# Kernel tuning notes

Measured on AMD Instinct MI355X. Metric: run time of the kernel, lower is better.

Reference implementation:

```python
import jax, jax.numpy as jnp
import numpy as np

B, N, D = 256, 400, 512
K = 20  # args.gcn_topk == self.k


def setup_inputs() -> dict:
    key = jax.random.key(0)
    k1, k2, k3, k4 = jax.random.split(key, 4)
    node_embs = jax.random.normal(k1, (B, N, D), dtype=jnp.float32)
    h_t = jax.random.normal(k2, (B, D), dtype=jnp.float32)
    mask = jnp.ones((B, N), dtype=jnp.float32)  # unused by forward, kept for signature fidelity
    # mapper = Linear(rnn_dim=512, gcn_dim=512) followed by Tanh
    lim = 1.0 / np.sqrt(D)
    W_map = jax.random.uniform(k3, (D, D), dtype=jnp.float32, minval=-lim, maxval=lim)
    b_map = jax.random.uniform(k4, (D,), dtype=jnp.float32, minval=-lim, maxval=lim)
    return {"node_embs": node_embs, "mask": mask, "h_t": h_t, "W_map": W_map, "b_map": b_map}


def reference(node_embs, mask, h_t, W_map, b_map):
    # scorer = Tanh(Linear(h_t.detach()))  -> [B, D]
    scorer = jnp.tanh(jax.lax.stop_gradient(h_t) @ W_map.T + b_map)
    # scores = bmm(node_embs, scorer) / ||scorer||  -> [B, N]
    scores = jnp.einsum('bnd,bd->bn', node_embs, scorer)
    scores = scores / jnp.linalg.norm(scorer, axis=1, keepdims=True)
    # top-k over nodes
    vals, topk_indices = jax.lax.top_k(scores, K)  # [B, K]
    # vals are always finite => topk_indices_out == topk_indices;
    # repeat_num = K/K + 1 = 2, then truncated back to K => no-op
    topk_indices_out = topk_indices
    # gather rows topk_indices; the original expand(-1,-1,gcn_topk) selects only
    # the FIRST K feature columns -> out is [B, K, K]
    gathered = jnp.take_along_axis(node_embs[:, :, :K], topk_indices[:, :, None], axis=1)
    tanh_s = jnp.tanh(jnp.take_along_axis(scores, topk_indices, axis=1))  # [B, K]
    out = gathered * tanh_s[:, :, None]  # [B, K, K]
    # softmax over nodes, entropy of the categorical, log-prob gather
    logp = jax.nn.log_softmax(scores, axis=1)  # [B, N]
    probs = jnp.exp(logp)
    entropy_object = -jnp.sum(probs * logp, axis=1)  # [B]
    score = jnp.take_along_axis(logp, topk_indices, axis=-1)  # [B, K]
    policy_score = jnp.mean(score, axis=1)  # [B]
    return (jnp.swapaxes(out, 1, 2), policy_score, scorer, entropy_object, topk_indices_out)
```

## Files before the change

kernel.cpp:

```cpp
#include <hip/hip_runtime.h>
#include <math.h>
#include <float.h>

#define BB 256
#define NN 400
#define DD 512
#define KK 20

__device__ __forceinline__ float dot8(float4 a0, float4 a1, float4 b0, float4 b1) {
    return a0.x*b0.x + a0.y*b0.y + a0.z*b0.z + a0.w*b0.w
         + a1.x*b1.x + a1.y*b1.y + a1.z*b1.z + a1.w*b1.w;
}

__global__ __launch_bounds__(1024) void scorer_kernel(
    const float* __restrict__ h_t,
    const float* __restrict__ W,
    const float* __restrict__ bmap,
    float* __restrict__ out2)
{
    const int blk = blockIdx.x;
    const int dc = blk & 15, bg = blk >> 4;
    const int wave = threadIdx.x >> 6, lane = threadIdx.x & 63;

    const int d0 = dc * 32 + wave * 2;
    const int d1 = d0 + 1;
    const float4* wp0 = (const float4*)(W + (size_t)d0 * DD);
    const float4* wp1 = (const float4*)(W + (size_t)d1 * DD);
    const float4 w00 = wp0[lane], w01 = wp0[lane + 64];
    const float4 w10 = wp1[lane], w11 = wp1[lane + 64];
    const float bias0 = bmap[d0], bias1 = bmap[d1];

    #pragma unroll 4
    for (int bi = 0; bi < 32; ++bi) {
        const int b = bg * 32 + bi;
        const float4* hp = (const float4*)(h_t + (size_t)b * DD);
        float4 hb0 = hp[lane], hb1 = hp[lane + 64];
        float p0 = dot8(w00, w01, hb0, hb1);
        float p1 = dot8(w10, w11, hb0, hb1);
        #pragma unroll
        for (int off = 32; off; off >>= 1) {
            p0 += __shfl_xor(p0, off, 64);
            p1 += __shfl_xor(p1, off, 64);
        }
        if (lane == 0) {
            out2[(size_t)b * DD + d0] = tanhf(p0 + bias0);
            out2[(size_t)b * DD + d1] = tanhf(p1 + bias1);
        }
    }
}

__global__ __launch_bounds__(1024, 4) void fused_topk_kernel(
    const float* __restrict__ embs,
    const float* __restrict__ scorer,
    float* __restrict__ out0,
    float* __restrict__ out1,
    float* __restrict__ out3,
    float* __restrict__ out4)
{
    const int b = blockIdx.x;
    const int t = threadIdx.x;
    const int wave = t >> 6, lane = t & 63;

    __shared__ float sh_sc[DD];
    __shared__ float sh_s[NN];
    __shared__ float redf[16], redf2[16], redq[8];
    __shared__ float mZ[3];
    __shared__ int   sh_topk[KK];
    __shared__ float sh_th[KK];

    if (t < DD) {
        float v = scorer[(size_t)b * DD + t];
        sh_sc[t] = v;
        float ss = v * v;
        #pragma unroll
        for (int off = 32; off; off >>= 1) ss += __shfl_xor(ss, off, 64);
        if (lane == 0) redq[wave] = ss;
    }
    __syncthreads();

    const float4 g0 = ((const float4*)sh_sc)[lane];
    const float4 g1 = ((const float4*)sh_sc)[lane + 64];

    {
        const int n0 = wave * 25;
        const float* base = embs + ((size_t)b * NN + n0) * DD;

        float4 A0[5], A1[5], B0[5], B1[5];
        #pragma unroll
        for (int r = 0; r < 5; ++r) {
            const float4* p = (const float4*)(base + (size_t)r * DD);
            A0[r] = p[lane]; A1[r] = p[lane + 64];
        }
        #pragma unroll
        for (int g = 0; g < 5; ++g) {
            if (g < 4) {
                #pragma unroll
                for (int r = 0; r < 5; ++r) {
                    const float4* p = (const float4*)(base + (size_t)((g + 1) * 5 + r) * DD);
                    B0[r] = p[lane]; B1[r] = p[lane + 64];
                }
            }
            float s[5];
            #pragma unroll
            for (int r = 0; r < 5; ++r) s[r] = dot8(A0[r], A1[r], g0, g1);
            #pragma unroll
            for (int off = 32; off; off >>= 1) {
                #pragma unroll
                for (int r = 0; r < 5; ++r) s[r] += __shfl_xor(s[r], off, 64);
            }
            if (lane == 0) {
                float* o = sh_s + n0 + g * 5;
                #pragma unroll
                for (int r = 0; r < 5; ++r) o[r] = s[r];
            }
            if (g < 4) {
                #pragma unroll
                for (int r = 0; r < 5; ++r) { A0[r] = B0[r]; A1[r] = B1[r]; }
            }
        }
    }
    __syncthreads();

    if (t == 0) {
        float tot = 0.f;
        #pragma unroll
        for (int i = 0; i < 8; ++i) tot += redq[i];
        mZ[0] = 1.0f / sqrtf(tot);
    }
    __syncthreads();
    const float inv = mZ[0];

    const float x = (t < NN) ? sh_s[t] * inv : -FLT_MAX;
    {
        float m = x;
        #pragma unroll
        for (int off = 32; off; off >>= 1) m = fmaxf(m, __shfl_xor(m, off, 64));
        if (lane == 0) redf[wave] = m;
    }
    __syncthreads();
    if (t == 0) {
        float m = redf[0];
        #pragma unroll
        for (int i = 1; i < 16; ++i) m = fmaxf(m, redf[i]);
        mZ[1] = m;
    }
    __syncthreads();
    const float m = mZ[1];

    {
        float e = 0.f, wv = 0.f;
        if (t < NN) {
            float d = x - m;
            e = expf(d);
            wv = e * d;
        }
        #pragma unroll
        for (int off = 32; off; off >>= 1) {
            e  += __shfl_xor(e, off, 64);
            wv += __shfl_xor(wv, off, 64);
        }
        if (lane == 0) { redf[wave] = e; redf2[wave] = wv; }
    }
    __syncthreads();
    if (t == 0) {
        float Z = 0.f, Ws = 0.f;
        #pragma unroll
        for (int i = 0; i < 16; ++i) { Z += redf[i]; Ws += redf2[i]; }
        float logZ = logf(Z);
        mZ[2] = logZ;
        out3[b] = logZ - Ws / Z;
    }
    __syncthreads();
    const float logZ = mZ[2];

    if (wave == 0) {
        float v0 = sh_s[lane      ] * inv;
        float v1 = sh_s[lane +  64] * inv;
        float v2 = sh_s[lane + 128] * inv;
        float v3 = sh_s[lane + 192] * inv;
        float v4 = sh_s[lane + 256] * inv;
        float v5 = sh_s[lane + 320] * inv;
        float v6 = (lane + 384 < NN) ? sh_s[lane + 384] * inv : -FLT_MAX;
        float acc = 0.f;
        for (int k = 0; k < KK; ++k) {
            float bv = v0; int bi = lane;
            if (v1 > bv) { bv = v1; bi = lane + 64; }
            if (v2 > bv) { bv = v2; bi = lane + 128; }
            if (v3 > bv) { bv = v3; bi = lane + 192; }
            if (v4 > bv) { bv = v4; bi = lane + 256; }
            if (v5 > bv) { bv = v5; bi = lane + 320; }
            if (v6 > bv) { bv = v6; bi = lane + 384; }
            #pragma unroll
            for (int off = 32; off; off >>= 1) {
                float ov = __shfl_xor(bv, off, 64);
                int   oi = __shfl_xor(bi, off, 64);
                if (ov > bv || (ov == bv && oi < bi)) { bv = ov; bi = oi; }
            }
            if (lane == 0) {
                sh_topk[k] = bi;
                sh_th[k] = tanhf(bv);
                out4[(size_t)b * KK + k] = (float)bi;
                acc += bv - m - logZ;
            }
            v0 = (bi == lane      ) ? -FLT_MAX : v0;
            v1 = (bi == lane +  64) ? -FLT_MAX : v1;
            v2 = (bi == lane + 128) ? -FLT_MAX : v2;
            v3 = (bi == lane + 192) ? -FLT_MAX : v3;
            v4 = (bi == lane + 256) ? -FLT_MAX : v4;
            v5 = (bi == lane + 320) ? -FLT_MAX : v5;
            v6 = (bi == lane + 384) ? -FLT_MAX : v6;
        }
        if (lane == 0) out1[b] = acc / (float)KK;
    }
    __syncthreads();

    if (t < NN) {
        int k = t / KK;
        int j = t - k * KK;
        float val = embs[((size_t)b * NN + sh_topk[k]) * DD + j] * sh_th[k];
        out0[(size_t)b * (KK * KK) + j * KK + k] = val;
    }
}

extern "C" void kernel_launch(void* const* d_in, const int* in_sizes, int n_in,
                              void* d_out, int out_size, void* d_ws, size_t ws_size,
                              hipStream_t stream) {
    const float* node_embs = (const float*)d_in[0];
    const float* h_t   = (const float*)d_in[2];
    const float* W_map = (const float*)d_in[3];
    const float* b_map = (const float*)d_in[4];
    (void)in_sizes; (void)n_in; (void)out_size; (void)d_ws; (void)ws_size;

    float* ob = (float*)d_out;
    float* out0 = ob;
    float* out1 = ob + 102400;
    float* out2 = ob + 102656;
    float* out3 = ob + 233728;
    float* out4 = ob + 233984;

    scorer_kernel<<<128, 1024, 0, stream>>>(h_t, W_map, b_map, out2);
    fused_topk_kernel<<<BB, 1024, 0, stream>>>(node_embs, out2,
                                               out0, out1, out3, out4);
}
```

Measured before the change: 73.45 us.

## Fuse scorer GEMV into topk kernel and overlap with async LDS prefetch

Drops the separate scorer kernel. Inside each block, half the waves compute the tanh(h_t·W^T+b) row for their batch directly into LDS, while the other half stream the first 64 embedding rows into 128KB of dynamic LDS with global_load_lds. The score loop then reads those rows from LDS and the rest from global memory, and the final gather also reads from LDS when it can. This saves a launch and the scorer round-trip through global memory, but every block now re-reads the full 1MB W matrix. The large LDS allocation also limits blocks per CU, and the register double-buffered prefetch of embedding rows is removed.

```diff
diff --git a/kernel.cpp b/kernel.cpp
--- a/kernel.cpp
+++ b/kernel.cpp
@@ -6,54 +6,27 @@
 #define NN 400
 #define DD 512
 #define KK 20
+#define SROWS 64
 
 __device__ __forceinline__ float dot8(float4 a0, float4 a1, float4 b0, float4 b1) {
     return a0.x*b0.x + a0.y*b0.y + a0.z*b0.z + a0.w*b0.w
          + a1.x*b1.x + a1.y*b1.y + a1.z*b1.z + a1.w*b1.w;
 }
 
-__global__ __launch_bounds__(1024) void scorer_kernel(
+__device__ __forceinline__ void gload_lds16(const float* g, float* l) {
+    __builtin_amdgcn_global_load_lds(
+        (const __attribute__((address_space(1))) void*)g,
+        (__attribute__((address_space(3))) void*)l, 16, 0, 0);
+}
+
+__global__ __launch_bounds__(1024, 4) void fused_topk_kernel(
+    const float* __restrict__ embs,
     const float* __restrict__ h_t,
     const float* __restrict__ W,
     const float* __restrict__ bmap,
-    float* __restrict__ out2)
-{
-    const int blk = blockIdx.x;
-    const int dc = blk & 15, bg = blk >> 4;
-    const int wave = threadIdx.x >> 6, lane = threadIdx.x & 63;
-
-    const int d0 = dc * 32 + wave * 2;
-    const int d1 = d0 + 1;
-    const float4* wp0 = (const float4*)(W + (size_t)d0 * DD);
-    const float4* wp1 = (const float4*)(W + (size_t)d1 * DD);
-    const float4 w00 = wp0[lane], w01 = wp0[lane + 64];
-    const float4 w10 = wp1[lane], w11 = wp1[lane + 64];
-    const float bias0 = bmap[d0], bias1 = bmap[d1];
-
-    #pragma unroll 4
-    for (int bi = 0; bi < 32; ++bi) {
-        const int b = bg * 32 + bi;
-        const float4* hp = (const float4*)(h_t + (size_t)b * DD);
-        float4 hb0 = hp[lane], hb1 = hp[lane + 64];
-        float p0 = dot8(w00, w01, hb0, hb1);
-        float p1 = dot8(w10, w11, hb0, hb1);
-        #pragma unroll
-        for (int off = 32; off; off >>= 1) {
-            p0 += __shfl_xor(p0, off, 64);
-            p1 += __shfl_xor(p1, off, 64);
-        }
-        if (lane == 0) {
-            out2[(size_t)b * DD + d0] = tanhf(p0 + bias0);
-            out2[(size_t)b * DD + d1] = tanhf(p1 + bias1);
-        }
-    }
-}
-
-__global__ __launch_bounds__(1024, 4) void fused_topk_kernel(
-    const float* __restrict__ embs,
-    const float* __restrict__ scorer,
     float* __restrict__ out0,
     float* __restrict__ out1,
+    float* __restrict__ out2,
     float* __restrict__ out3,
     float* __restrict__ out4)
 {
@@ -61,6 +34,7 @@
     const int t = threadIdx.x;
     const int wave = t >> 6, lane = t & 63;
 
+    extern __shared__ float sh_rows[];
     __shared__ float sh_sc[DD];
     __shared__ float sh_s[NN];
     __shared__ float redf[16], redf2[16], redq[8];
@@ -68,15 +42,51 @@
     __shared__ int   sh_topk[KK];
     __shared__ float sh_th[KK];
 
+    if (wave < 8) {
+        const float4* hp = (const float4*)(h_t + (size_t)b * DD);
+        const float4 h0 = hp[lane], h1 = hp[lane + 64];
+        const int dbase = wave * 64;
+        #pragma unroll 4
+        for (int p = 0; p < 32; ++p) {
+            const int d0 = dbase + 2 * p, d1 = d0 + 1;
+            const float4* wp0 = (const float4*)(W + (size_t)d0 * DD);
+            const float4* wp1 = (const float4*)(W + (size_t)d1 * DD);
+            float4 a0 = wp0[lane], a1 = wp0[lane + 64];
+            float4 c0 = wp1[lane], c1 = wp1[lane + 64];
+            float s0 = dot8(a0, a1, h0, h1);
+            float s1 = dot8(c0, c1, h0, h1);
+            #pragma unroll
+            for (int off = 32; off; off >>= 1) {
+                s0 += __shfl_xor(s0, off, 64);
+                s1 += __shfl_xor(s1, off, 64);
+            }
+            if (lane == 0) {
+                sh_sc[d0] = tanhf(s0 + bmap[d0]);
+                sh_sc[d1] = tanhf(s1 + bmap[d1]);
+            }
+        }
+    } else {
+        const int ws = wave - 8;
+        const float* gbase = embs + ((size_t)b * NN + ws * 8) * DD;
+        #pragma unroll
+        for (int r = 0; r < 8; ++r) {
+            const float* grow = gbase + (size_t)r * DD + lane * 4;
+            float* lrow = sh_rows + (size_t)(ws * 8 + r) * DD;
+            gload_lds16(grow,            lrow);
+            gload_lds16(grow + 256,      lrow + 256);
+        }
+        asm volatile("s_waitcnt vmcnt(0)" ::: "memory");
+    }
+    __syncthreads();
+
     if (t < DD) {
-        float v = scorer[(size_t)b * DD + t];
-        sh_sc[t] = v;
+        float v = sh_sc[t];
+        out2[(size_t)b * DD + t] = v;
         float ss = v * v;
         #pragma unroll
         for (int off = 32; off; off >>= 1) ss += __shfl_xor(ss, off, 64);
         if (lane == 0) redq[wave] = ss;
     }
-    __syncthreads();
 
     const float4 g0 = ((const float4*)sh_sc)[lane];
     const float4 g1 = ((const float4*)sh_sc)[lane + 64];
@@ -84,20 +94,17 @@
     {
         const int n0 = wave * 25;
         const float* base = embs + ((size_t)b * NN + n0) * DD;
-
-        float4 A0[5], A1[5], B0[5], B1[5];
-        #pragma unroll
-        for (int r = 0; r < 5; ++r) {
-            const float4* p = (const float4*)(base + (size_t)r * DD);
-            A0[r] = p[lane]; A1[r] = p[lane + 64];
-        }
-        #pragma unroll
         for (int g = 0; g < 5; ++g) {
-            if (g < 4) {
-                #pragma unroll
-                for (int r = 0; r < 5; ++r) {
-                    const float4* p = (const float4*)(base + (size_t)((g + 1) * 5 + r) * DD);
-                    B0[r] = p[lane]; B1[r] = p[lane + 64];
+            float4 A0[5], A1[5];
+            #pragma unroll
+            for (int r = 0; r < 5; ++r) {
+                const int row = n0 + g * 5 + r;
+                if (row < SROWS) {
+                    const float4* lp = (const float4*)(sh_rows + (size_t)row * DD);
+                    A0[r] = lp[lane]; A1[r] = lp[lane + 64];
+                } else {
+                    const float4* p = (const float4*)(base + (size_t)(g * 5 + r) * DD);
+                    A0[r] = p[lane]; A1[r] = p[lane + 64];
                 }
             }
             float s[5];
@@ -112,10 +119,6 @@
                 float* o = sh_s + n0 + g * 5;
                 #pragma unroll
                 for (int r = 0; r < 5; ++r) o[r] = s[r];
-            }
-            if (g < 4) {
-                #pragma unroll
-                for (int r = 0; r < 5; ++r) { A0[r] = B0[r]; A1[r] = B1[r]; }
             }
         }
     }
@@ -217,7 +220,9 @@
     if (t < NN) {
         int k = t / KK;
         int j = t - k * KK;
-        float val = embs[((size_t)b * NN + sh_topk[k]) * DD + j] * sh_th[k];
+        int row = sh_topk[k];
+        float val = (row < SROWS ? sh_rows[(size_t)row * DD + j]
+                                 : embs[((size_t)b * NN + row) * DD + j]) * sh_th[k];
         out0[(size_t)b * (KK * KK) + j * KK + k] = val;
     }
 }
@@ -238,7 +243,7 @@
     float* out3 = ob + 233728;
     float* out4 = ob + 233984;
 
-    scorer_kernel<<<128, 1024, 0, stream>>>(h_t, W_map, b_map, out2);
-    fused_topk_kernel<<<BB, 1024, 0, stream>>>(node_embs, out2,
-                                               out0, out1, out3, out4);
-}
+    const size_t dyn_lds = (size_t)SROWS * DD * sizeof(float);
+    fused_topk_kernel<<<BB, 1024, dyn_lds, stream>>>(
+        node_embs, h_t, W_map, b_map, out0, out1, out2, out3, out4);
+}
```

Measured after the change: 74.16 us. No clear change (+1.0%).
